# Kernel tuning notes

Hardware: AMD Instinct MI355X
Metric: run time of the kernel (lower is better)

The kernel has to match this reference:

```python
import jax, jax.numpy as jnp
import numpy as np

DIMS = [1536, 2048, 2560, 3072, 1792, 2304, 2816, 2048, 2560, 3328]

def _ln(x, g, b, eps=1e-5):
    m = jnp.mean(x, -1, keepdims=True)
    v = jnp.mean((x - m) ** 2, -1, keepdims=True)
    return (x - m) / jnp.sqrt(v + eps) * g + b

def _gelu(x):
    return jax.nn.gelu(x, approximate=False)

def _mish(x):
    return x * jnp.tanh(jax.nn.softplus(x))

_ACTS = [jax.nn.silu, _gelu, _mish, jax.nn.relu, jax.nn.selu, jnp.tanh, jax.nn.softplus, jax.nn.elu]

def _renorm_sparse_topk(probs, active_k, max_k):
    vals, idx = jax.lax.top_k(probs, max_k)
    mask = (jnp.arange(max_k)[None, :] < active_k[:, None]).astype(probs.dtype)
    n = probs.shape[0]
    sparse = jnp.zeros_like(probs).at[jnp.arange(n)[:, None], idx].set(vals * mask)
    return sparse / jnp.clip(jnp.sum(sparse, -1, keepdims=True), 1e-6, None)

def setup_inputs():
    N, IN, OUT, E, M, S, SUB, DST, INNER, SH = 2048, 1024, 10, 10, 24, 4, 4, 40, 768, 2048
    DMAX = max(DIMS)
    ks = iter(jax.random.split(jax.random.key(0), 80))
    def p(shape, std=0.02):
        return jax.random.normal(next(ks), shape, jnp.float32) * std
    eu = np.zeros((E, DMAX, IN), np.float32)
    ed = np.zeros((E, OUT, DMAX), np.float32)
    for i in range(E):
        d = DIMS[i % len(DIMS)]
        eu[i, :d] = np.asarray(p((d, IN), 0.02))
        ed[i, :, :d] = np.asarray(p((OUT, d), 0.01))
    return {
        'x': jax.random.normal(next(ks), (N, IN), jnp.float32),
        'weight': p((OUT, IN), 0.03), 'bias': p((OUT,), 0.01),
        'shared_up_w': p((SH, IN)), 'shared_down_w': p((OUT, SH), 0.01),
        'shared_norm_g': jnp.ones((OUT,)), 'shared_norm_b': jnp.zeros((OUT,)),
        'shared_scale': jnp.asarray(1.0, jnp.float32),
        'memory_keys': p((M, IN)), 'memory_values_init': p((M, IN)),
        'memory_query_w': p((IN, IN), 0.01), 'memory_out_w': p((OUT, IN), 0.01),
        'mem_wgate_w': p((M, 2 * IN), 0.01), 'mem_wgate_b': jnp.zeros((M,)),
        'mem_wval_w': p((IN, IN), 0.01), 'mem_wval_b': jnp.zeros((IN,)),
        'depth_q_w': p((IN, IN), 0.01), 'depth_k_w': p((IN, IN), 0.01),
        'depth_v_w': p((IN, IN), 0.01), 'depth_out_w': p((OUT, IN), 0.01),
        'cell_ln_g': jnp.ones((S, IN)), 'cell_ln_b': jnp.zeros((S, IN)),
        'cell_fc1_w': p((S, INNER, IN)), 'cell_fc1_b': jnp.zeros((S, INNER)),
        'cell_fc2_w': p((S, IN, INNER)), 'cell_fc2_b': jnp.zeros((S, IN)),
        'ssm_a_w': p((DST, IN), 0.01), 'ssm_a_b': jnp.zeros((DST,)),
        'ssm_b_w': p((IN, DST), 0.01), 'ssm_b_b': jnp.zeros((IN,)),
        'mor_sub_w': p((SUB, E, IN)), 'mor_sub_b': jnp.zeros((SUB, E)),
        'mor_mix_w': p((SUB, IN)), 'mor_mix_b': jnp.zeros((SUB,)),
        'expert_bias': jnp.zeros((E,)),
        'budget_w': p((4, IN)), 'budget_b': jnp.zeros((4,)),
        'experts_up': jnp.asarray(eu), 'experts_down': jnp.asarray(ed),
        'expert_norm_g': jnp.ones((E, OUT)), 'expert_norm_b': jnp.zeros((E, OUT)),
        'halt_w': p((S, 1, IN), 0.01), 'halt_b': jnp.full((S, 1), -2.0, jnp.float32),
        'alpha': jnp.asarray(0.1, jnp.float32), 'beta': jnp.asarray(0.1, jnp.float32),
    }

def reference(x, weight, bias, shared_up_w, shared_down_w, shared_norm_g, shared_norm_b, shared_scale, memory_keys, memory_values_init, memory_query_w, memory_out_w, mem_wgate_w, mem_wgate_b, mem_wval_w, mem_wval_b, depth_q_w, depth_k_w, depth_v_w, depth_out_w, cell_ln_g, cell_ln_b, cell_fc1_w, cell_fc1_b, cell_fc2_w, cell_fc2_b, ssm_a_w, ssm_a_b, ssm_b_w, ssm_b_b, mor_sub_w, mor_sub_b, mor_mix_w, mor_mix_b, expert_bias, budget_w, budget_b, experts_up, experts_down, expert_norm_g, expert_norm_b, halt_w, halt_b, alpha, beta):
    in_dim = x.shape[-1]
    x_flat = x.reshape(-1, in_dim)
    n = x_flat.shape[0]
    base = x_flat @ weight.T + bias
    shared = _ln(jax.nn.silu(x_flat @ shared_up_w.T) @ shared_down_w.T, shared_norm_g, shared_norm_b)
    mem_vals = jnp.broadcast_to(memory_values_init[None], (n,) + memory_values_init.shape)
    current = x_flat
    total = jnp.zeros_like(base)
    cum_halt = jnp.zeros((n, 1), x.dtype)
    bank = []
    mem_scale = in_dim ** -0.5
    steps = cell_ln_g.shape[0]
    n_exp = expert_bias.shape[0]
    max_topk = min(4, n_exp)
    for step in range(steps):
        mq = current @ memory_query_w.T
        mem_attn = jax.nn.softmax((mq @ memory_keys.T) * mem_scale, -1)  # [n, M]
        mem_ctx = jnp.einsum('nm,nmd->nd', mem_attn, mem_vals)
        if bank:
            ds = jnp.stack(bank, 1)  # [n, s, d]
            q = current @ depth_q_w.T
            k = ds @ depth_k_w.T
            v = ds @ depth_v_w.T
            attn = jax.nn.softmax(jnp.einsum('nd,nsd->ns', q, k) * mem_scale, -1)
            depth_ctx = jnp.einsum('ns,nsd->nd', attn, v)
        else:
            depth_ctx = jnp.zeros_like(current)
        ssm_corr = jnp.tanh(current @ ssm_a_w.T + ssm_a_b) @ ssm_b_w.T + ssm_b_b
        enriched = current + 0.34 * mem_ctx + 0.22 * depth_ctx + 0.18 * ssm_corr
        h = _gelu(_ln(enriched, cell_ln_g[step], cell_ln_b[step]) @ cell_fc1_w[step].T + cell_fc1_b[step])
        current = enriched + h @ cell_fc2_w[step].T + cell_fc2_b[step]
        bank.append(current)
        sub = jnp.einsum('nd,sed->nse', current, mor_sub_w) + mor_sub_b[None]
        mix = jax.nn.softmax(current @ mor_mix_w.T + mor_mix_b, -1)
        gate_probs = jax.nn.softmax(jnp.einsum('ns,nse->ne', mix, sub) + expert_bias, -1)
        budget = 1 + jnp.argmax(jax.nn.softmax(current @ budget_w.T + budget_b, -1), -1)
        sg = _renorm_sparse_topk(gate_probs, budget, max_topk)
        expert_logits = jnp.zeros_like(base)
        for i in range(n_exp):
            d = DIMS[i % len(DIMS)]
            hh = _ACTS[i % len(_ACTS)](current @ experts_up[i, :d, :].T)
            eo = _ln(hh @ experts_down[i, :, :d].T, expert_norm_g[i], expert_norm_b[i])
            expert_logits = expert_logits + sg[:, i:i + 1] * eo
        step_logits = expert_logits + 0.22 * (mem_ctx @ memory_out_w.T) + 0.14 * (depth_ctx @ depth_out_w.T)
        surprise = 1.0 - jnp.max(sg, -1, keepdims=True)  # [n, 1]
        wg = jax.nn.softmax(jnp.concatenate([current, mem_ctx], -1) @ mem_wgate_w.T + mem_wgate_b, -1)
        wv = (current @ mem_wval_w.T + mem_wval_b)[:, None, :]
        mem_vals = mem_vals + surprise[..., None] * wg[..., None] * (wv - mem_vals)
        halt = jax.nn.sigmoid((current + 0.2 * mem_ctx + 0.1 * depth_ctx) @ halt_w[step].T + halt_b[step])
        remaining = 1.0 - cum_halt
        total = total + remaining * step_logits
        cum_halt = cum_halt + remaining * halt
    total = total / float(steps)
    out = base + shared_scale * shared + (alpha + 1e-4) * total + beta * (current @ memory_out_w.T)
    return out.reshape(x.shape[:-1] + (out.shape[-1],))
```

## Files before the change

### kernel.cpp

```cpp
#include <hip/hip_runtime.h>
#include <stdint.h>

#define N_TOK 2048
#define IN_D  1024
#define NEXP  10
#define NSTEP 4
#define INNER 768
#define SHD   2048
#define DMAX  3328
#define DSUM  24064

typedef __attribute__((ext_vector_type(4))) float f32x4;
typedef __attribute__((ext_vector_type(8))) short bf16x8;

__device__ const int c_dims[10] = {1536,2048,2560,3072,1792,2304,2816,2048,2560,3328};
__device__ const int c_offs[10] = {0,1536,3584,6144,9216,11008,13312,16128,18176,20736};
__device__ const int c_acts[10] = {0,1,2,3,4,5,6,7,0,1};
__device__ const int c_cum[11]  = {0,12,28,48,72,86,104,126,142,162,188};

__device__ __forceinline__ float wred(float v){
#pragma unroll
  for (int s = 32; s > 0; s >>= 1) v += __shfl_xor(v, s, 64);
  return v;
}
__device__ __forceinline__ float wmax(float v){
#pragma unroll
  for (int s = 32; s > 0; s >>= 1) v = fmaxf(v, __shfl_xor(v, s, 64));
  return v;
}
__device__ __forceinline__ float bf2f(uint16_t u){
  return __uint_as_float(((uint32_t)u) << 16);
}
__device__ __forceinline__ uint16_t f2bf(float f){
  uint32_t u = __float_as_uint(f);
  return (uint16_t)((u + 0x7FFFu + ((u >> 16) & 1u)) >> 16);
}
__device__ __forceinline__ uint8_t f2fp8(float f){
  uint32_t u = __float_as_uint(f);
  uint8_t sign = (uint8_t)((u >> 24) & 0x80u);
  uint32_t absu = u & 0x7FFFFFFFu;
  if (absu >= 0x43E00000u) return sign | 0x7Eu;
  if (absu < 0x3C800000u){
    float af = __uint_as_float(absu);
    int q = (int)rintf(af * 512.0f);
    return sign | (uint8_t)q;
  }
  uint32_t mant = absu & 0x7FFFFFu;
  uint32_t exp = absu >> 23;
  uint32_t lsb = (mant >> 20) & 1u;
  uint32_t rounded = mant + 0x7FFFFu + lsb;
  if (rounded >= 0x800000u){ exp += 1; rounded = 0; }
  uint32_t e8 = exp - 120;
  uint32_t m8 = (rounded >> 20) & 7u;
  if (e8 > 15u || (e8 == 15u && m8 == 7u)) return sign | 0x7Eu;
  return sign | (uint8_t)((e8 << 3) | m8);
}
__device__ __forceinline__ void gload16(const uint16_t* g, uint16_t* l){
  __builtin_amdgcn_global_load_lds(
      (const __attribute__((address_space(1))) uint32_t*)(const void*)g,
      (__attribute__((address_space(3))) uint32_t*)(void*)l, 16, 0, 0);
}
__device__ __forceinline__ void gload16b(const void* g, void* l){
  __builtin_amdgcn_global_load_lds(
      (const __attribute__((address_space(1))) uint32_t*)g,
      (__attribute__((address_space(3))) uint32_t*)l, 16, 0, 0);
}

__device__ __forceinline__ float actf(int a, float x){
  switch(a){
    case 0: return x / (1.f + expf(-x));
    case 1: return 0.5f * x * (1.f + erff(x * 0.7071067811865475f));
    case 2: { float sp = fmaxf(x,0.f) + log1pf(expf(-fabsf(x)));
              return x * tanhf(sp); }
    case 3: return fmaxf(x, 0.f);
    case 4: return x > 0.f ? 1.0507009873554805f * x
                           : 1.7580993408473768f * expm1f(x);
    case 5: return tanhf(x);
    case 6: return fmaxf(x,0.f) + log1pf(expf(-fabsf(x)));
    default: return x > 0.f ? x : expm1f(x);
  }
}

__global__ void split_kernel(const float* __restrict__ src, uint16_t* __restrict__ hi,
                             uint16_t* __restrict__ lo, size_t n){
  size_t i = ((size_t)blockIdx.x * blockDim.x + threadIdx.x) << 2;
  size_t stride = ((size_t)gridDim.x * blockDim.x) << 2;
  for (; i < n; i += stride){
    float4 v = *(const float4*)(src + i);
    ushort4 h, l;
    h.x = f2bf(v.x); l.x = f2bf(v.x - bf2f(h.x));
    h.y = f2bf(v.y); l.y = f2bf(v.y - bf2f(h.y));
    h.z = f2bf(v.z); l.z = f2bf(v.z - bf2f(h.z));
    h.w = f2bf(v.w); l.w = f2bf(v.w - bf2f(h.w));
    *(ushort4*)(hi + i) = h;
    *(ushort4*)(lo + i) = l;
  }
}
__global__ void split_strided(const float* __restrict__ src, uint16_t* __restrict__ hi,
                              uint16_t* __restrict__ lo, int rows, int cols, int ldd){
  int nq = rows * (cols >> 2);
  for (int i = blockIdx.x * blockDim.x + threadIdx.x; i < nq; i += gridDim.x * blockDim.x){
    int r = i / (cols >> 2), c4 = (i - r * (cols >> 2)) << 2;
    float4 v = *(const float4*)(src + (size_t)r * cols + c4);
    ushort4 h, l;
    h.x = f2bf(v.x); l.x = f2bf(v.x - bf2f(h.x));
    h.y = f2bf(v.y); l.y = f2bf(v.y - bf2f(h.y));
    h.z = f2bf(v.z); l.z = f2bf(v.z - bf2f(h.z));
    h.w = f2bf(v.w); l.w = f2bf(v.w - bf2f(h.w));
    size_t d = (size_t)r * ldd + c4;
    *(ushort4*)(hi + d) = h;
    *(ushort4*)(lo + d) = l;
  }
}
__global__ void cvt_fp8_kernel(const float* __restrict__ src, uint8_t* __restrict__ dst, size_t n){
  size_t i = ((size_t)blockIdx.x * blockDim.x + threadIdx.x) << 2;
  size_t stride = ((size_t)gridDim.x * blockDim.x) << 2;
  for (; i < n; i += stride){
    float4 v = *(const float4*)(src + i);
    uchar4 q;
    q.x = f2fp8(v.x); q.y = f2fp8(v.y); q.z = f2fp8(v.z); q.w = f2fp8(v.w);
    *(uchar4*)(dst + i) = q;
  }
}
__global__ void fill1_kernel(float* __restrict__ p, int n){
  int i = blockIdx.x * blockDim.x + threadIdx.x;
  if (i < n) p[i] = 1.f;
}
__global__ void tr_sbw_kernel(const float* __restrict__ src, float* __restrict__ dst){
  int i = blockIdx.x * 256 + threadIdx.x;
  if (i < 40 * 1024){
    int o = i >> 10, d = i & 1023;
    dst[i] = src[d * 40 + o];
  }
}

__global__ __launch_bounds__(256)
void k2_kernel(const float* __restrict__ keys, const float* __restrict__ mqw,
               float* __restrict__ K2){
  int m = blockIdx.x;
  int j = blockIdx.y * 256 + threadIdx.x;
  float acc = 0.f;
  for (int d = 0; d < 1024; d++)
    acc = fmaf(keys[m * 1024 + d], mqw[d * 1024 + j], acc);
  K2[m * 1024 + j] = acc;
}

__global__ void build_routew(const float* __restrict__ msw, const float* __restrict__ mmw,
                             const float* __restrict__ bw, const float* __restrict__ wgw,
                             const float* __restrict__ hw, const float* __restrict__ mow,
                             const float* __restrict__ dow, uint16_t* __restrict__ Wh,
                             uint16_t* __restrict__ Wl){
  const int TOT = 4 * 128 * 3072;
  for (int i = blockIdx.x * 256 + threadIdx.x; i < TOT; i += gridDim.x * 256){
    int t = i / (128 * 3072);
    int rem = i - t * (128 * 3072);
    int row = rem / 3072, col = rem - row * 3072;
    float v = 0.f;
    if (row < 40){ if (col < 1024) v = msw[row * 1024 + col]; }
    else if (row < 44){ if (col < 1024) v = mmw[(row - 40) * 1024 + col]; }
    else if (row < 48){ if (col < 1024) v = bw[(row - 44) * 1024 + col]; }
    else if (row < 72){ if (col < 2048) v = wgw[(row - 48) * 2048 + col]; }
    else if (row == 72){
      if (col < 1024) v = hw[t * 1024 + col];
      else if (col < 2048) v = 0.2f * hw[t * 1024 + col - 1024];
      else v = 0.1f * hw[t * 1024 + col - 2048];
    }
    else if (row < 83){ if (col >= 1024 && col < 2048) v = mow[(row - 73) * 1024 + col - 1024]; }
    else if (row < 93){ if (col >= 2048) v = dow[(row - 83) * 1024 + col - 2048]; }
    else if (row < 103){ if (col < 1024) v = mow[(row - 93) * 1024 + col]; }
    uint16_t h = f2bf(v);
    Wh[i] = h; Wl[i] = f2bf(v - bf2f(h));
  }
}

enum { EPI_GELU=0, EPI_CUR=1, EPI_PRE=2, EPI_QROUTE=3 };

template<int EPI>
__global__ __launch_bounds__(256)
void gemm_sp(const uint16_t* __restrict__ Ah, const uint16_t* __restrict__ Al, int lda,
             const uint16_t* __restrict__ Wh, const uint16_t* __restrict__ Wl,
             const uint16_t* __restrict__ W2h, const uint16_t* __restrict__ W2l,
             const float* __restrict__ bias, const float* __restrict__ addend,
             float* __restrict__ D0, float* __restrict__ D1, float* __restrict__ D2,
             float* __restrict__ D3, uint8_t* __restrict__ o8,
             uint16_t* __restrict__ oH, uint16_t* __restrict__ oL,
             int K, int D)
{
  __shared__ __align__(16) uint16_t sm[4][2][4096];
  int tid = threadIdx.x, lane = tid & 63, wave = tid >> 6;
  int wr = wave >> 1, wc = wave & 1;
  int arow = lane & 15, agrp = lane >> 4;
  int rowBase = blockIdx.y * 128;
  bool isRoute = (EPI == EPI_QROUTE) && ((int)blockIdx.x < 4);
  const uint16_t* Wsh = isRoute ? W2h : Wh;
  const uint16_t* Wsl = isRoute ? W2l : Wl;
  int wst     = isRoute ? 3072 : K;
  int colBase = isRoute ? 0 : ((EPI == EPI_QROUTE ? (int)blockIdx.x - 4 : (int)blockIdx.x) * 128);
  int kBase   = isRoute ? (int)blockIdx.x * 768 : 0;
  int kLen    = isRoute ? 768 : K;
  f32x4 acc[4][4];
#pragma unroll
  for (int m = 0; m < 4; m++)
#pragma unroll
    for (int n = 0; n < 4; n++){ f32x4 z = {0.f,0.f,0.f,0.f}; acc[m][n] = z; }

#define STAGE_G(buf, k0) do { \
  _Pragma("unroll") \
  for (int s = 0; s < 2; s++){ \
    int u = tid + s * 256; \
    int rr = u >> 2; \
    int ch = (u & 3) ^ ((rr >> 1) & 3); \
    size_t ga = (size_t)(rowBase + rr) * lda + kBase + (k0) + ch * 8; \
    size_t gw = (size_t)(colBase + rr) * wst + kBase + (k0) + ch * 8; \
    gload16(&Ah[ga], &sm[0][buf][u << 3]); \
    gload16(&Al[ga], &sm[1][buf][u << 3]); \
    gload16(&Wsh[gw], &sm[2][buf][u << 3]); \
    gload16(&Wsl[gw], &sm[3][buf][u << 3]); \
  } } while(0)

  int nk = kLen >> 5;
  STAGE_G(0, 0);
  if (nk > 1) STAGE_G(1, 32);
  int perm = (arow >> 1) & 3;
#pragma unroll 1
  for (int ki = 0; ki < nk; ki++){
    int cb = ki & 1;
    if (ki + 1 < nk) asm volatile("s_waitcnt vmcnt(8)" ::: "memory");
    else             asm volatile("s_waitcnt vmcnt(0)" ::: "memory");
    __builtin_amdgcn_s_barrier();
    bf16x8 ah[4], al[4], bh[4], bl[4];
#pragma unroll
    for (int m = 0; m < 4; m++){
      int u = ((wr*64 + m*16 + arow) << 2) + (agrp ^ perm);
      ah[m] = *(const bf16x8*)&sm[0][cb][u << 3];
      al[m] = *(const bf16x8*)&sm[1][cb][u << 3];
    }
#pragma unroll
    for (int n = 0; n < 4; n++){
      int u = ((wc*64 + n*16 + arow) << 2) + (agrp ^ perm);
      bh[n] = *(const bf16x8*)&sm[2][cb][u << 3];
      bl[n] = *(const bf16x8*)&sm[3][cb][u << 3];
    }
#pragma unroll
    for (int m = 0; m < 4; m++)
#pragma unroll
      for (int n = 0; n < 4; n++){
        acc[m][n] = __builtin_amdgcn_mfma_f32_16x16x32_bf16(ah[m], bh[n], acc[m][n], 0, 0, 0);
        acc[m][n] = __builtin_amdgcn_mfma_f32_16x16x32_bf16(ah[m], bl[n], acc[m][n], 0, 0, 0);
        acc[m][n] = __builtin_amdgcn_mfma_f32_16x16x32_bf16(al[m], bh[n], acc[m][n], 0, 0, 0);
      }
    __builtin_amdgcn_s_barrier();
    asm volatile("" ::: "memory");
    if (ki + 2 < nk) STAGE_G(cb, (ki + 2) << 5);
  }
#undef STAGE_G
#pragma unroll
  for (int m = 0; m < 4; m++){
#pragma unroll
    for (int n = 0; n < 4; n++){
      int col = colBase + wc*64 + n*16 + arow;
#pragma unroll
      for (int r2 = 0; r2 < 4; r2++){
        int row = rowBase + wr*64 + m*16 + agrp*4 + r2;
        float v = acc[m][n][r2];
        if (EPI == EPI_GELU){
          v += bias[col];
          v = 0.5f * v * (1.f + erff(v * 0.7071067811865475f));
          size_t idx = (size_t)row * D + col;
          uint16_t h = f2bf(v); oH[idx] = h; oL[idx] = f2bf(v - bf2f(h));
        }
        if (EPI == EPI_CUR){
          v += bias[col] + addend[(size_t)row * 1024 + col];
          D0[(size_t)row * 1024 + col] = v;
          size_t idx = (size_t)row * 3072 + col;
          uint16_t h = f2bf(v); oH[idx] = h; oL[idx] = f2bf(v - bf2f(h));
          o8[(size_t)row * 1024 + col] = f2fp8(v);
        }
        if (EPI == EPI_PRE){
          if (col < 2048) D0[(size_t)row * 2048 + col] = v / (1.f + expf(-v));
          else D1[(size_t)row * 128 + col - 2048] = v;
        }
        if (EPI == EPI_QROUTE){
          if (isRoute){
            D3[((size_t)blockIdx.x * N_TOK + row) * 128 + col] = v;
          } else {
            if (col < 1024) D0[(size_t)row * 1024 + col] = v;
            else if (col < 4096) D1[(size_t)row * 3072 + col - 1024] = v + bias[col - 1024];
            else if (col < 4160) D2[(size_t)row * 128 + col - 4096] = v;
          }
        }
      }
    }
  }
}

__global__ __launch_bounds__(256)
void expert_up_mfma(const uint8_t* __restrict__ A8, const uint8_t* __restrict__ U8,
                    const int* __restrict__ cnt, const int* __restrict__ gidx,
                    uint16_t* __restrict__ HH)
{
  int bid = blockIdx.x;
  int ex = bid / 192;
  int ey = bid - ex * 192;
  if (ey >= 188) return;
  int e = 0;
#pragma unroll
  for (int i = 1; i < 11; i++) if (ey >= c_cum[i]) e = i;
  int ct = ey - c_cum[e];
  int dcols = c_dims[e];
  int ne = cnt[e];
  const uint8_t* W = U8 + (size_t)e * DMAX * IN_D + (size_t)ct * 128 * IN_D;

  __shared__ __align__(16) uint8_t smem[32768];
  int tid = threadIdx.x, lane = tid & 63, wave = tid >> 6;
  int wr = wave >> 1, wc = wave & 1;
  int arow = lane & 15, agrp = lane >> 4;
  int actid = c_acts[e];
  size_t base_e = (size_t)N_TOK * c_offs[e];
  int rHalf = tid >> 1;
  int h16 = (((tid & 1) ^ ((tid >> 3) & 1)) << 4);
  int off = ((((agrp >> 1) ^ ((arow >> 2) & 1)) << 4) | ((agrp & 1) << 3));

#define STAGE_E(b, k0) do { \
    gload16b(&A8[(size_t)tok * IN_D + (k0) + h16], &smem[(b)*8192 + tid*16]); \
    gload16b(&W[(size_t)rHalf * IN_D + (k0) + h16], &smem[(b)*8192 + 4096 + tid*16]); \
  } while(0)

#pragma unroll 1
  for (int rowBase = ex * 128; rowBase < ne; rowBase += 4 * 128){
    int slot = rowBase + rHalf;
    int tok = (slot < ne) ? gidx[e * N_TOK + slot] : 0;

    f32x4 acc[4][4];
#pragma unroll
    for (int m = 0; m < 4; m++)
#pragma unroll
      for (int n = 0; n < 4; n++){ f32x4 z = {0.f,0.f,0.f,0.f}; acc[m][n] = z; }

    STAGE_E(0, 0);
    STAGE_E(1, 32);
    STAGE_E(2, 64);
    int cb = 0;
#pragma unroll 1
    for (int ki = 0; ki < 32; ki++){
      if (ki < 30)       asm volatile("s_waitcnt vmcnt(4)" ::: "memory");
      else if (ki == 30) asm volatile("s_waitcnt vmcnt(2)" ::: "memory");
      else               asm volatile("s_waitcnt vmcnt(0)" ::: "memory");
      __builtin_amdgcn_s_barrier();
      long a[4], b[4];
#pragma unroll
      for (int m = 0; m < 4; m++)
        a[m] = *(const long*)&smem[cb*8192 + (wr*64 + m*16 + arow)*32 + off];
#pragma unroll
      for (int n = 0; n < 4; n++)
        b[n] = *(const long*)&smem[cb*8192 + 4096 + (wc*64 + n*16 + arow)*32 + off];
#pragma unroll
      for (int m = 0; m < 4; m++)
#pragma unroll
        for (int n = 0; n < 4; n++)
          acc[m][n] = __builtin_amdgcn_mfma_f32_16x16x32_fp8_fp8(a[m], b[n], acc[m][n], 0, 0, 0);
      __builtin_amdgcn_s_barrier();
      asm volatile("" ::: "memory");
      if (ki + 3 < 32) STAGE_E(cb, (ki + 3) << 5);
      cb = (cb == 2) ? 0 : cb + 1;
    }
    uint16_t* Ht = (uint16_t*)smem;
#pragma unroll
    for (int m = 0; m < 4; m++){
      int rb0 = wr*64 + m*16 + agrp*4;
#pragma unroll
      for (int n = 0; n < 4; n++){
        int col = wc*64 + n*16 + arow;
#pragma unroll
        for (int r2 = 0; r2 < 4; r2++){
          int row = rb0 + r2;
          float v = actf(actid, acc[m][n][r2]);
          Ht[row * 128 + (col ^ ((row & 7) << 3))] = f2bf(v);
        }
      }
    }
    __syncthreads();
#pragma unroll
    for (int i = 0; i < 8; i++){
      int c = tid + i * 256;
      int row = c >> 4, chunk = c & 15;
      int schunk = (chunk & 8) | ((chunk ^ row) & 7);
      int4 val = *(const int4*)&Ht[row * 128 + schunk * 8];
      *(int4*)&HH[base_e + (size_t)(rowBase + row) * dcols
                  + (size_t)ct * 128 + chunk * 8] = val;
    }
    __syncthreads();
  }
#undef STAGE_E
}

__global__ __launch_bounds__(256)
void ctx_enr_kernel(const float* __restrict__ qaux, const float* __restrict__ dqbuf,
                    const float* __restrict__ Ac, const float* __restrict__ W0,
                    const float* __restrict__ W1, const float* __restrict__ W2,
                    const float* __restrict__ mvi,
                    const float* __restrict__ t0, const float* __restrict__ t1,
                    const float* __restrict__ t2, const float* __restrict__ cur,
                    const float* __restrict__ sab, const float* __restrict__ sbwT,
                    const float* __restrict__ sbb, const float* __restrict__ lng,
                    const float* __restrict__ lnbv,
                    float* __restrict__ enr, uint16_t* __restrict__ lnh,
                    uint16_t* __restrict__ lnl, uint16_t* __restrict__ Arh,
                    uint16_t* __restrict__ Arl, int t)
{
  int row = blockIdx.x, tid = threadIdx.x;
  __shared__ float su[24], ss[3], s40[40], red[12], redm[8];
  if (tid < 64){
    float pj = (tid < 24) ? qaux[(size_t)row * 128 + tid] * 0.03125f : -1e30f;
    float mx = wmax(pj);
    float ex = (tid < 24) ? expf(pj - mx) : 0.f;
    float sum = wred(ex);
    float attn = ex / sum;
    if (tid < 24) su[tid] = attn * Ac[row * 24 + tid];
    float w0v = (t > 0 && tid < 24) ? W0[row * 24 + tid] : 0.f;
    float s0 = wred(attn * w0v);
    float w1v = (t > 1 && tid < 24) ? W1[row * 24 + tid] : 0.f;
    float s1 = wred(attn * w1v);
    float w2v = (t > 2 && tid < 24) ? W2[row * 24 + tid] : 0.f;
    float s2 = wred(attn * w2v);
    if (tid == 0){ ss[0] = s0; ss[1] = s1; ss[2] = s2; }
    if (tid < 40) s40[tid] = tanhf(qaux[(size_t)row * 128 + 24 + tid] + sab[tid]);
  }
  size_t tb = (size_t)row * 3072;
  if (t > 0){
    float a0 = 0.f, a1 = 0.f, a2 = 0.f;
#pragma unroll
    for (int j = 0; j < 4; j++){
      int d = tid + j * 256;
      float dq = dqbuf[(size_t)row * 1024 + d];
      a0 = fmaf(dq, t0[tb + d], a0);
      if (t > 1) a1 = fmaf(dq, t1[tb + d], a1);
      if (t > 2) a2 = fmaf(dq, t2[tb + d], a2);
    }
    a0 = wred(a0); a1 = wred(a1); a2 = wred(a2);
    if ((tid & 63) == 0){ int w = tid >> 6; red[w] = a0; red[4+w] = a1; red[8+w] = a2; }
  }
  __syncthreads();
  float e0 = 0.f, e1 = 0.f, e2 = 0.f;
  if (t > 0){
    float A0 = (red[0]+red[1]+red[2]+red[3]) * 0.03125f;
    float A1 = (red[4]+red[5]+red[6]+red[7]) * 0.03125f;
    float A2 = (red[8]+red[9]+red[10]+red[11]) * 0.03125f;
    float dmx = A0;
    if (t > 1) dmx = fmaxf(dmx, A1);
    if (t > 2) dmx = fmaxf(dmx, A2);
    e0 = expf(A0 - dmx);
    e1 = (t > 1) ? expf(A1 - dmx) : 0.f;
    e2 = (t > 2) ? expf(A2 - dmx) : 0.f;
    float dinv = 1.f / (e0 + e1 + e2);
    e0 *= dinv; e1 *= dinv; e2 *= dinv;
  }
  size_t ar = (size_t)row * 3072;
  float ev[4];
  float part = 0.f;
#pragma unroll
  for (int j = 0; j < 4; j++){
    int d = tid + j * 256;
    size_t idx = (size_t)row * IN_D + d;
    float mv = 0.f;
#pragma unroll
    for (int m = 0; m < 24; m++) mv = fmaf(su[m], mvi[m * IN_D + d], mv);
    float dv = 0.f;
    if (t > 0){
      mv = fmaf(ss[0], t0[tb + 2048 + d], mv);
      dv = e0 * t0[tb + 1024 + d];
      if (t > 1){ mv = fmaf(ss[1], t1[tb + 2048 + d], mv); dv = fmaf(e1, t1[tb + 1024 + d], dv); }
      if (t > 2){ mv = fmaf(ss[2], t2[tb + 2048 + d], mv); dv = fmaf(e2, t2[tb + 1024 + d], dv); }
    }
    float sv = sbb[d];
#pragma unroll
    for (int o = 0; o < 40; o++) sv = fmaf(s40[o], sbwT[o * 1024 + d], sv);
    float v = cur[idx] + 0.34f * mv + 0.22f * dv + 0.18f * sv;
    uint16_t mh = f2bf(mv);
    Arh[ar + 1024 + d] = mh; Arl[ar + 1024 + d] = f2bf(mv - bf2f(mh));
    uint16_t dh = f2bf(dv);
    Arh[ar + 2048 + d] = dh; Arl[ar + 2048 + d] = f2bf(dv - bf2f(dh));
    ev[j] = v; part += v;
  }
  part = wred(part);
  if ((tid & 63) == 0) redm[tid >> 6] = part;
  __syncthreads();
  float mean = (redm[0] + redm[1] + redm[2] + redm[3]) * (1.f / 1024.f);
  float vp = 0.f;
#pragma unroll
  for (int j = 0; j < 4; j++){ float dd = ev[j] - mean; vp += dd * dd; }
  vp = wred(vp);
  if ((tid & 63) == 0) redm[4 + (tid >> 6)] = vp;
  __syncthreads();
  float var = (redm[4] + redm[5] + redm[6] + redm[7]) * (1.f / 1024.f);
  float rs = 1.f / sqrtf(var + 1e-5f);
#pragma unroll
  for (int j = 0; j < 4; j++){
    int d = tid + j * 256;
    size_t idx = (size_t)row * IN_D + d;
    enr[idx] = ev[j];
    float v = (ev[j] - mean) * rs * lng[t * IN_D + d] + lnbv[t * IN_D + d];
    uint16_t h = f2bf(v);
    lnh[idx] = h;
    lnl[idx] = f2bf(v - bf2f(h));
  }
}

__global__ __launch_bounds__(256)
void route_fin(const float* __restrict__ ROq, const float* __restrict__ mmb,
               const float* __restrict__ msb, const float* __restrict__ ebias,
               const float* __restrict__ bb, const float* __restrict__ wgb,
               const float* __restrict__ hb,
               float* __restrict__ sg, float* __restrict__ haltb,
               float* __restrict__ Ac, float* __restrict__ W0,
               float* __restrict__ W1, float* __restrict__ W2,
               int* __restrict__ cnt, int* __restrict__ gidx,
               int* __restrict__ pos, float* __restrict__ routeS, int t)
{
  int row = blockIdx.x * 256 + threadIdx.x;
  int lane = threadIdx.x & 63;
  const size_t P = (size_t)N_TOK * 128;
  const float* r0 = ROq + (size_t)row * 128;
  const float* r1 = r0 + P;
  const float* r2 = r0 + 2 * P;
  const float* r3 = r0 + 3 * P;
  auto R = [&](int j){ return r0[j] + r1[j] + r2[j] + r3[j]; };
  float pm[4];
#pragma unroll
  for (int o = 0; o < 4; o++) pm[o] = R(40 + o) + mmb[o];
  float mmx = fmaxf(fmaxf(pm[0], pm[1]), fmaxf(pm[2], pm[3]));
  float msum = 0.f;
#pragma unroll
  for (int o = 0; o < 4; o++){ pm[o] = expf(pm[o] - mmx); msum += pm[o]; }
  float minv = 1.f / msum;
  float gl[10];
#pragma unroll
  for (int e = 0; e < 10; e++){
    float g = ebias[e];
#pragma unroll
    for (int s2 = 0; s2 < 4; s2++)
      g = fmaf(pm[s2] * minv, R(s2 * 10 + e) + msb[s2 * 10 + e], g);
    gl[e] = g;
  }
  float gmx = gl[0];
#pragma unroll
  for (int e = 1; e < 10; e++) gmx = fmaxf(gmx, gl[e]);
  float gs = 0.f;
#pragma unroll
  for (int e = 0; e < 10; e++){ gl[e] = expf(gl[e] - gmx); gs += gl[e]; }
  float ginv = 1.f / gs;
#pragma unroll
  for (int e = 0; e < 10; e++) gl[e] *= ginv;
  float pb0 = R(44) + bb[0], pb1 = R(45) + bb[1], pb2 = R(46) + bb[2], pb3 = R(47) + bb[3];
  int bud = 1; float bbest = pb0;
  if (pb1 > bbest){ bbest = pb1; bud = 2; }
  if (pb2 > bbest){ bbest = pb2; bud = 3; }
  if (pb3 > bbest){ bbest = pb3; bud = 4; }
  float tv[4]; int ti[4]; unsigned used = 0;
#pragma unroll
  for (int j = 0; j < 4; j++){
    float best = -1e30f; int bi = 0;
#pragma unroll
    for (int e = 0; e < 10; e++){
      bool ok = (!((used >> e) & 1u)) && (gl[e] > best);
      if (ok){ best = gl[e]; bi = e; }
    }
    tv[j] = best; ti[j] = bi; used |= (1u << bi);
  }
  float ssum = tv[0];
  if (bud > 1) ssum += tv[1];
  if (bud > 2) ssum += tv[2];
  if (bud > 3) ssum += tv[3];
  float den = fmaxf(ssum, 1e-6f);
  float sup = 1.f - tv[0] / den;
  float sgv[10];
#pragma unroll
  for (int e = 0; e < 10; e++){
    float sv = 0.f;
#pragma unroll
    for (int j = 0; j < 4; j++) if (j < bud && ti[j] == e) sv = tv[j] / den;
    sgv[e] = sv;
    sg[row * 10 + e] = sv;
  }
  float pw[24];
#pragma unroll
  for (int m = 0; m < 24; m++) pw[m] = R(48 + m) + wgb[m];
  float wmx2 = pw[0];
#pragma unroll
  for (int m = 1; m < 24; m++) wmx2 = fmaxf(wmx2, pw[m]);
  float wsum = 0.f;
#pragma unroll
  for (int m = 0; m < 24; m++){ pw[m] = expf(pw[m] - wmx2); wsum += pw[m]; }
  float winv = 1.f / wsum;
#pragma unroll
  for (int m = 0; m < 24; m++){
    float c = sup * pw[m] * winv;
    float om = 1.f - c;
    Ac[row * 24 + m] *= om;
    if (t > 0) W0[row * 24 + m] *= om;
    if (t > 1) W1[row * 24 + m] *= om;
    if (t > 2) W2[row * 24 + m] *= om;
    if (t == 0)      W0[row * 24 + m] = c;
    else if (t == 1) W1[row * 24 + m] = c;
    else if (t == 2) W2[row * 24 + m] = c;
  }
  haltb[row] = 1.f / (1.f + expf(-(R(72) + hb[t])));
#pragma unroll
  for (int i = 0; i < 30; i++) routeS[row * 32 + i] = R(73 + i);
#pragma unroll
  for (int e = 0; e < 10; e++){
    bool act = sgv[e] != 0.f;
    unsigned long long mask = __ballot(act);
    int cw = __popcll(mask);
    int b0 = 0;
    if (lane == 0 && cw > 0) b0 = atomicAdd(&cnt[e], cw);
    b0 = __shfl(b0, 0, 64);
    if (act){
      int slot = b0 + __popcll(mask & ((1ull << lane) - 1ull));
      gidx[e * N_TOK + slot] = row;
      pos[row * 10 + e] = slot;
    }
  }
}

__global__ __launch_bounds__(256)
void downfin_kernel(const uint16_t* __restrict__ HH, const int* __restrict__ pos,
                    const float* __restrict__ ED, const float* __restrict__ sg,
                    const float* __restrict__ eng, const float* __restrict__ enb,
                    const float* __restrict__ routeS, const float* __restrict__ haltb,
                    float* __restrict__ total, float* __restrict__ cumh)
{
  int lane = threadIdx.x & 63;
  int row = blockIdx.x * 4 + (threadIdx.x >> 6);
  float out[10] = {};
  for (int e = 0; e < NEXP; e++){
    float g = sg[row * 10 + e];
    if (g != 0.0f){
      int d = c_dims[e];
      int slot = pos[row * 10 + e];
      const uint16_t* hr = HH + (size_t)N_TOK * c_offs[e] + (size_t)slot * d;
      const float* wd = ED + (size_t)e * 10 * DMAX;
      float p[10] = {};
      for (int k = lane * 4; k < d; k += 256){
        uint2 hv = *(const uint2*)&hr[k];
        float h0 = bf2f((uint16_t)hv.x), h1 = bf2f((uint16_t)(hv.x >> 16));
        float h2 = bf2f((uint16_t)hv.y), h3 = bf2f((uint16_t)(hv.y >> 16));
#pragma unroll
        for (int o = 0; o < 10; o++){
          float4 w4 = *(const float4*)&wd[o * DMAX + k];
          p[o] = fmaf(h0, w4.x, fmaf(h1, w4.y, fmaf(h2, w4.z, fmaf(h3, w4.w, p[o]))));
        }
      }
#pragma unroll
      for (int o = 0; o < 10; o++) p[o] = wred(p[o]);
      float mean = 0.f;
#pragma unroll
      for (int o = 0; o < 10; o++) mean += p[o];
      mean *= 0.1f;
      float var = 0.f;
#pragma unroll
      for (int o = 0; o < 10; o++){ float dd = p[o] - mean; var += dd * dd; }
      var *= 0.1f;
      float rs = 1.f / sqrtf(var + 1e-5f);
#pragma unroll
      for (int o = 0; o < 10; o++)
        out[o] += g * ((p[o] - mean) * rs * eng[e * 10 + o] + enb[e * 10 + o]);
    }
  }
  if (lane == 0){
    const float* r = routeS + (size_t)row * 32;
    float rem = 1.f - cumh[row];
#pragma unroll
    for (int o = 0; o < 10; o++)
      total[row * 10 + o] += rem * (out[o] + 0.22f * r[o] + 0.14f * r[10 + o]);
    cumh[row] += rem * haltb[row];
  }
}

__global__ __launch_bounds__(256)
void shared_kernel(const float* __restrict__ shpre, const float* __restrict__ sdw,
                   const float* __restrict__ g, const float* __restrict__ b,
                   float* __restrict__ outp)
{
  int lane = threadIdx.x & 63;
  int row = blockIdx.x * 4 + (threadIdx.x >> 6);
  const float* xr = shpre + (size_t)row * SHD;
  float p[10];
#pragma unroll
  for (int o = 0; o < 10; o++) p[o] = 0.f;
  for (int k = lane; k < SHD; k += 64){
    float xv = xr[k];
#pragma unroll
    for (int o = 0; o < 10; o++) p[o] = fmaf(xv, sdw[o * SHD + k], p[o]);
  }
#pragma unroll
  for (int o = 0; o < 10; o++) p[o] = wred(p[o]);
  float mean = 0.f;
#pragma unroll
  for (int o = 0; o < 10; o++) mean += p[o];
  mean *= 0.1f;
  float var = 0.f;
#pragma unroll
  for (int o = 0; o < 10; o++){ float dd = p[o] - mean; var += dd * dd; }
  var *= 0.1f;
  float rs = 1.f / sqrtf(var + 1e-5f);
  if (lane == 0){
#pragma unroll
    for (int o = 0; o < 10; o++) outp[row * 10 + o] = (p[o] - mean) * rs * g[o] + b[o];
  }
}

__global__ __launch_bounds__(256)
void final_lite(const float* __restrict__ qaux, const float* __restrict__ biasp,
                const float* __restrict__ sharedp, const float* __restrict__ total,
                const float* __restrict__ routeS, const float* __restrict__ sscale,
                const float* __restrict__ alphap, const float* __restrict__ betap,
                float* __restrict__ outp)
{
  int row = blockIdx.x * 256 + threadIdx.x;
  float ss = sscale[0], av = alphap[0] + 1e-4f, bv = betap[0];
#pragma unroll
  for (int o = 0; o < 10; o++)
    outp[row * 10 + o] = (qaux[(size_t)row * 128 + 64 + o] + biasp[o])
                       + ss * sharedp[row * 10 + o]
                       + av * (total[row * 10 + o] * 0.25f)
                       + bv * routeS[(size_t)row * 32 + 20 + o];
}

extern "C" void kernel_launch(void* const* d_in, const int* in_sizes, int n_in,
                              void* d_out, int out_size, void* d_ws, size_t ws_size,
                              hipStream_t stream)
{
  const float* x     = (const float*)d_in[0];
  const float* wgt   = (const float*)d_in[1];
  const float* bias  = (const float*)d_in[2];
  const float* suw   = (const float*)d_in[3];
  const float* sdw   = (const float*)d_in[4];
  const float* sng   = (const float*)d_in[5];
  const float* snb   = (const float*)d_in[6];
  const float* sscale= (const float*)d_in[7];
  const float* keys  = (const float*)d_in[8];
  const float* mvi   = (const float*)d_in[9];
  const float* mqw   = (const float*)d_in[10];
  const float* mow   = (const float*)d_in[11];
  const float* wgw   = (const float*)d_in[12];
  const float* wgb   = (const float*)d_in[13];
  const float* wvw   = (const float*)d_in[14];
  const float* wvb   = (const float*)d_in[15];
  const float* dqw   = (const float*)d_in[16];
  const float* dkw   = (const float*)d_in[17];
  const float* dvw   = (const float*)d_in[18];
  const float* dow   = (const float*)d_in[19];
  const float* clng  = (const float*)d_in[20];
  const float* clnb  = (const float*)d_in[21];
  const float* fc1w  = (const float*)d_in[22];
  const float* fc1b  = (const float*)d_in[23];
  const float* fc2w  = (const float*)d_in[24];
  const float* fc2b  = (const float*)d_in[25];
  const float* saw   = (const float*)d_in[26];
  const float* sab   = (const float*)d_in[27];
  const float* sbw   = (const float*)d_in[28];
  const float* sbb   = (const float*)d_in[29];
  const float* msw   = (const float*)d_in[30];
  const float* msb   = (const float*)d_in[31];
  const float* mmw   = (const float*)d_in[32];
  const float* mmb   = (const float*)d_in[33];
  const float* ebias = (const float*)d_in[34];
  const float* bw    = (const float*)d_in[35];
  const float* bb    = (const float*)d_in[36];
  const float* eup   = (const float*)d_in[37];
  const float* edn   = (const float*)d_in[38];
  const float* eng   = (const float*)d_in[39];
  const float* enb   = (const float*)d_in[40];
  const float* hw    = (const float*)d_in[41];
  const float* hb    = (const float*)d_in[42];
  const float* alphap= (const float*)d_in[43];
  const float* betap = (const float*)d_in[44];
  float* outp = (float*)d_out;

  char* wsb = (char*)d_ws;
  size_t off = 0;
  auto AL = [&](size_t bytes) -> void* {
    void* p = wsb + off;
    off = (off + bytes + 255) & ~(size_t)255;
    return p;
  };
  const size_t NI = (size_t)N_TOK * IN_D;
  float* cur    = (float*)AL(NI * 4);
  float* enr    = (float*)AL(NI * 4);
  float* dqbuf  = (float*)AL(NI * 4);
  float* qaux   = (float*)AL((size_t)N_TOK * 128 * 4);
  float* routeQ = (float*)AL((size_t)4 * N_TOK * 128 * 4);
  float* routeS = (float*)AL((size_t)N_TOK * 32 * 4);
  float* trio0  = (float*)AL((size_t)N_TOK * 3072 * 4);
  float* trio1  = (float*)AL((size_t)N_TOK * 3072 * 4);
  float* trio2  = (float*)AL((size_t)N_TOK * 3072 * 4);
  float* Ac     = (float*)AL((size_t)N_TOK * 24 * 4);
  float* W0     = (float*)AL((size_t)N_TOK * 24 * 4);
  float* W1     = (float*)AL((size_t)N_TOK * 24 * 4);
  float* W2     = (float*)AL((size_t)N_TOK * 24 * 4);
  float* sg     = (float*)AL((size_t)N_TOK * 10 * 4);
  float* haltb  = (float*)AL((size_t)N_TOK * 4);
  char*  zblk   = (char*)AL((size_t)N_TOK * 10 * 4 + N_TOK * 4 + 4 * 16 * 4);
  float* total  = (float*)zblk;
  float* cumh   = (float*)(zblk + (size_t)N_TOK * 10 * 4);
  int*   cnt    = (int*)(zblk + (size_t)N_TOK * 10 * 4 + N_TOK * 4);
  int*   gidx   = (int*)AL((size_t)NEXP * N_TOK * 4);
  int*   pos    = (int*)AL((size_t)N_TOK * NEXP * 4);
  float* sharedp= (float*)AL((size_t)N_TOK * 10 * 4);
  float* cbias  = (float*)AL(3072 * 4);
  float* K2f    = (float*)AL((size_t)24 * 1024 * 4);
  float* sbwT   = (float*)AL((size_t)40 * 1024 * 4);
  uint16_t* lnh  = (uint16_t*)AL(NI * 2);
  uint16_t* lnl  = (uint16_t*)AL(NI * 2);
  uint16_t* h7h  = (uint16_t*)AL((size_t)N_TOK * INNER * 2);
  uint16_t* h7l  = (uint16_t*)AL((size_t)N_TOK * INNER * 2);
  uint16_t* Arh  = (uint16_t*)AL((size_t)N_TOK * 3072 * 2);
  uint16_t* Arl  = (uint16_t*)AL((size_t)N_TOK * 3072 * 2);
  const size_t W1M = (size_t)IN_D * IN_D;
  uint16_t* preWh  = (uint16_t*)AL((size_t)2176 * 1024 * 2);
  uint16_t* preWl  = (uint16_t*)AL((size_t)2176 * 1024 * 2);
  uint16_t* qtWh   = (uint16_t*)AL((size_t)4224 * 1024 * 2);
  uint16_t* qtWl   = (uint16_t*)AL((size_t)4224 * 1024 * 2);
  uint16_t* rtWh   = (uint16_t*)AL((size_t)4 * 128 * 3072 * 2);
  uint16_t* rtWl   = (uint16_t*)AL((size_t)4 * 128 * 3072 * 2);
  const size_t WFC = (size_t)NSTEP * INNER * IN_D;
  uint16_t* fc1wh = (uint16_t*)AL(WFC * 2); uint16_t* fc1wl = (uint16_t*)AL(WFC * 2);
  uint16_t* fc2wh = (uint16_t*)AL(WFC * 2); uint16_t* fc2wl = (uint16_t*)AL(WFC * 2);
  uint8_t* upbf8 = (uint8_t*)AL((size_t)NEXP * DMAX * IN_D);
  uint8_t* A8    = (uint8_t*)AL(NI);
  uint16_t* HHc  = (uint16_t*)AL((size_t)N_TOK * DSUM * 2);
  float* shpre  = (float*)HHc;

  hipMemsetAsync(zblk, 0, (size_t)N_TOK * 10 * 4 + N_TOK * 4 + 4 * 16 * 4, stream);
  hipMemsetAsync(cbias, 0, 3072 * 4, stream);
  hipMemcpyAsync(cbias + 2048, wvb, 1024 * 4, hipMemcpyDeviceToDevice, stream);
  hipMemcpyAsync(cur, x, NI * 4, hipMemcpyDeviceToDevice, stream);
  fill1_kernel<<<(N_TOK * 24 + 255) / 256, 256, 0, stream>>>(Ac, N_TOK * 24);
  cvt_fp8_kernel<<<2048, 256, 0, stream>>>(eup, upbf8, (size_t)NEXP * DMAX * IN_D);
  tr_sbw_kernel<<<160, 256, 0, stream>>>(sbw, sbwT);

  split_strided<<<1024, 256, 0, stream>>>(x, Arh, Arl, N_TOK, 1024, 3072);
  split_kernel<<<1024, 256, 0, stream>>>(suw, preWh, preWl, (size_t)SHD * 1024);
  split_kernel<<<256, 256, 0, stream>>>(saw, preWh + (size_t)2072*1024, preWl + (size_t)2072*1024, (size_t)40 * 1024);
  split_kernel<<<256, 256, 0, stream>>>(wgt, preWh + (size_t)2112*1024, preWl + (size_t)2112*1024, (size_t)10 * 1024);
  hipMemsetAsync(preWh + (size_t)2122*1024, 0, (size_t)54 * 1024 * 2, stream);
  hipMemsetAsync(preWl + (size_t)2122*1024, 0, (size_t)54 * 1024 * 2, stream);
  split_kernel<<<1024, 256, 0, stream>>>(dqw, qtWh, qtWl, W1M);
  split_kernel<<<1024, 256, 0, stream>>>(dkw, qtWh + W1M, qtWl + W1M, W1M);
  split_kernel<<<1024, 256, 0, stream>>>(dvw, qtWh + 2*W1M, qtWl + 2*W1M, W1M);
  split_kernel<<<1024, 256, 0, stream>>>(wvw, qtWh + 3*W1M, qtWl + 3*W1M, W1M);
  split_kernel<<<256, 256, 0, stream>>>(saw, qtWh + (size_t)4120*1024, qtWl + (size_t)4120*1024, (size_t)40 * 1024);
  hipMemsetAsync(qtWh + (size_t)4160*1024, 0, (size_t)64 * 1024 * 2, stream);
  hipMemsetAsync(qtWl + (size_t)4160*1024, 0, (size_t)64 * 1024 * 2, stream);
  k2_kernel<<<dim3(24, 4), 256, 0, stream>>>(keys, mqw, K2f);
  split_kernel<<<256, 256, 0, stream>>>(K2f, preWh + (size_t)2048*1024, preWl + (size_t)2048*1024, (size_t)24 * 1024);
  split_kernel<<<256, 256, 0, stream>>>(K2f, qtWh + (size_t)4096*1024, qtWl + (size_t)4096*1024, (size_t)24 * 1024);
  build_routew<<<2048, 256, 0, stream>>>(msw, mmw, bw, wgw, hw, mow, dow, rtWh, rtWl);
  split_kernel<<<1024, 256, 0, stream>>>(fc1w, fc1wh, fc1wl, WFC);
  split_kernel<<<1024, 256, 0, stream>>>(fc2w, fc2wh, fc2wl, WFC);

  gemm_sp<EPI_PRE><<<dim3(17, 16), 256, 0, stream>>>(
      Arh, Arl, 3072, preWh, preWl, nullptr, nullptr, nullptr, nullptr,
      shpre, qaux, nullptr, nullptr, nullptr, nullptr, nullptr, IN_D, 2176);
  shared_kernel<<<512, 256, 0, stream>>>(shpre, sdw, sng, snb, sharedp);

  float* trioB[3] = {trio0, trio1, trio2};

  for (int t = 0; t < NSTEP; t++){
    ctx_enr_kernel<<<2048, 256, 0, stream>>>(qaux, dqbuf, Ac, W0, W1, W2, mvi,
                                             trio0, trio1, trio2, cur, sab, sbwT, sbb,
                                             clng, clnb, enr, lnh, lnl, Arh, Arl, t);
    gemm_sp<EPI_GELU><<<dim3(INNER/128, 16), 256, 0, stream>>>(
        lnh, lnl, 1024, fc1wh + (size_t)t * INNER * IN_D, fc1wl + (size_t)t * INNER * IN_D,
        nullptr, nullptr, fc1b + t * INNER, nullptr,
        nullptr, nullptr, nullptr, nullptr, nullptr, h7h, h7l, IN_D, INNER);
    gemm_sp<EPI_CUR><<<dim3(8, 16), 256, 0, stream>>>(
        h7h, h7l, 768, fc2wh + (size_t)t * IN_D * INNER, fc2wl + (size_t)t * IN_D * INNER,
        nullptr, nullptr, fc2b + t * IN_D, enr,
        cur, nullptr, nullptr, nullptr, A8, Arh, Arl, INNER, IN_D);
    gemm_sp<EPI_QROUTE><<<dim3(t < 3 ? 37 : 4, 16), 256, 0, stream>>>(
        Arh, Arl, 3072, qtWh, qtWl,
        rtWh + (size_t)t * 128 * 3072, rtWl + (size_t)t * 128 * 3072,
        cbias, nullptr, dqbuf, t < 3 ? trioB[t] : nullptr, qaux, routeQ,
        nullptr, nullptr, nullptr, IN_D, 4224);
    route_fin<<<8, 256, 0, stream>>>(routeQ, mmb, msb, ebias, bb, wgb, hb,
                                     sg, haltb, Ac, W0, W1, W2,
                                     cnt + t * 16, gidx, pos, routeS, t);
    expert_up_mfma<<<768, 256, 0, stream>>>(A8, upbf8, cnt + t * 16, gidx, HHc);
    downfin_kernel<<<512, 256, 0, stream>>>(HHc, pos, edn, sg, eng, enb,
                                            routeS, haltb, total, cumh);
  }
  final_lite<<<8, 256, 0, stream>>>(qaux, bias, sharedp, total, routeS,
                                    sscale, alphap, betap, outp);
}
```

Measured before the change: 2.076 ms.

## Process four rows per block in ctx_enr to reuse memory-value and side weights

The context-enrichment kernel now handles four token rows per 256-thread block, with one wave per row for the softmax and depth-attention scalars. Each loaded element of mvi and sbwT feeds four rows, so the shared weight reads drop to a quarter. Per-row values are staged in a 16 KB shared buffer for the layernorm pass. The cost is fewer blocks (512 instead of 2048) and more shared memory per block, which may lower occupancy and latency hiding in a kernel that is a small part of total time.

```diff
diff --git a/kernel.cpp b/kernel.cpp
--- a/kernel.cpp
+++ b/kernel.cpp
@@ -408,101 +408,133 @@
                     uint16_t* __restrict__ lnl, uint16_t* __restrict__ Arh,
                     uint16_t* __restrict__ Arl, int t)
 {
-  int row = blockIdx.x, tid = threadIdx.x;
-  __shared__ float su[24], ss[3], s40[40], red[12], redm[8];
-  if (tid < 64){
-    float pj = (tid < 24) ? qaux[(size_t)row * 128 + tid] * 0.03125f : -1e30f;
+  int row0 = blockIdx.x * 4;
+  int tid = threadIdx.x, lane = tid & 63, wave = tid >> 6;
+  int roww = row0 + wave;
+  __shared__ float su[4][24], ss[4][3], de[4][3], s40[4][40], redm[4][8];
+  __shared__ float sev[4][1024];
+  {
+    float pj = (lane < 24) ? qaux[(size_t)roww * 128 + lane] * 0.03125f : -1e30f;
     float mx = wmax(pj);
-    float ex = (tid < 24) ? expf(pj - mx) : 0.f;
+    float ex = (lane < 24) ? expf(pj - mx) : 0.f;
     float sum = wred(ex);
     float attn = ex / sum;
-    if (tid < 24) su[tid] = attn * Ac[row * 24 + tid];
-    float w0v = (t > 0 && tid < 24) ? W0[row * 24 + tid] : 0.f;
+    if (lane < 24) su[wave][lane] = attn * Ac[roww * 24 + lane];
+    float w0v = (t > 0 && lane < 24) ? W0[roww * 24 + lane] : 0.f;
     float s0 = wred(attn * w0v);
-    float w1v = (t > 1 && tid < 24) ? W1[row * 24 + tid] : 0.f;
+    float w1v = (t > 1 && lane < 24) ? W1[roww * 24 + lane] : 0.f;
     float s1 = wred(attn * w1v);
-    float w2v = (t > 2 && tid < 24) ? W2[row * 24 + tid] : 0.f;
+    float w2v = (t > 2 && lane < 24) ? W2[roww * 24 + lane] : 0.f;
     float s2 = wred(attn * w2v);
-    if (tid == 0){ ss[0] = s0; ss[1] = s1; ss[2] = s2; }
-    if (tid < 40) s40[tid] = tanhf(qaux[(size_t)row * 128 + 24 + tid] + sab[tid]);
-  }
-  size_t tb = (size_t)row * 3072;
+    if (lane == 0){ ss[wave][0] = s0; ss[wave][1] = s1; ss[wave][2] = s2; }
+    if (lane < 40) s40[wave][lane] = tanhf(qaux[(size_t)roww * 128 + 24 + lane] + sab[lane]);
+  }
   if (t > 0){
+    size_t tbw = (size_t)roww * 3072;
     float a0 = 0.f, a1 = 0.f, a2 = 0.f;
-#pragma unroll
-    for (int j = 0; j < 4; j++){
-      int d = tid + j * 256;
-      float dq = dqbuf[(size_t)row * 1024 + d];
-      a0 = fmaf(dq, t0[tb + d], a0);
-      if (t > 1) a1 = fmaf(dq, t1[tb + d], a1);
-      if (t > 2) a2 = fmaf(dq, t2[tb + d], a2);
-    }
-    a0 = wred(a0); a1 = wred(a1); a2 = wred(a2);
-    if ((tid & 63) == 0){ int w = tid >> 6; red[w] = a0; red[4+w] = a1; red[8+w] = a2; }
-  }
+    for (int d = lane; d < 1024; d += 64){
+      float dq = dqbuf[(size_t)roww * 1024 + d];
+      a0 = fmaf(dq, t0[tbw + d], a0);
+      if (t > 1) a1 = fmaf(dq, t1[tbw + d], a1);
+      if (t > 2) a2 = fmaf(dq, t2[tbw + d], a2);
+    }
+    a0 = wred(a0) * 0.03125f; a1 = wred(a1) * 0.03125f; a2 = wred(a2) * 0.03125f;
+    float dmx = a0;
+    if (t > 1) dmx = fmaxf(dmx, a1);
+    if (t > 2) dmx = fmaxf(dmx, a2);
+    float e0 = expf(a0 - dmx);
+    float e1 = (t > 1) ? expf(a1 - dmx) : 0.f;
+    float e2 = (t > 2) ? expf(a2 - dmx) : 0.f;
+    float dinv = 1.f / (e0 + e1 + e2);
+    if (lane == 0){ de[wave][0] = e0 * dinv; de[wave][1] = e1 * dinv; de[wave][2] = e2 * dinv; }
+  } else if (lane == 0){ de[wave][0] = 0.f; de[wave][1] = 0.f; de[wave][2] = 0.f; }
   __syncthreads();
-  float e0 = 0.f, e1 = 0.f, e2 = 0.f;
-  if (t > 0){
-    float A0 = (red[0]+red[1]+red[2]+red[3]) * 0.03125f;
-    float A1 = (red[4]+red[5]+red[6]+red[7]) * 0.03125f;
-    float A2 = (red[8]+red[9]+red[10]+red[11]) * 0.03125f;
-    float dmx = A0;
-    if (t > 1) dmx = fmaxf(dmx, A1);
-    if (t > 2) dmx = fmaxf(dmx, A2);
-    e0 = expf(A0 - dmx);
-    e1 = (t > 1) ? expf(A1 - dmx) : 0.f;
-    e2 = (t > 2) ? expf(A2 - dmx) : 0.f;
-    float dinv = 1.f / (e0 + e1 + e2);
-    e0 *= dinv; e1 *= dinv; e2 *= dinv;
-  }
-  size_t ar = (size_t)row * 3072;
-  float ev[4];
-  float part = 0.f;
-#pragma unroll
+  float part0 = 0.f, part1 = 0.f, part2 = 0.f, part3 = 0.f;
+#pragma unroll 1
   for (int j = 0; j < 4; j++){
     int d = tid + j * 256;
-    size_t idx = (size_t)row * IN_D + d;
-    float mv = 0.f;
-#pragma unroll
-    for (int m = 0; m < 24; m++) mv = fmaf(su[m], mvi[m * IN_D + d], mv);
-    float dv = 0.f;
-    if (t > 0){
-      mv = fmaf(ss[0], t0[tb + 2048 + d], mv);
-      dv = e0 * t0[tb + 1024 + d];
-      if (t > 1){ mv = fmaf(ss[1], t1[tb + 2048 + d], mv); dv = fmaf(e1, t1[tb + 1024 + d], dv); }
-      if (t > 2){ mv = fmaf(ss[2], t2[tb + 2048 + d], mv); dv = fmaf(e2, t2[tb + 1024 + d], dv); }
-    }
-    float sv = sbb[d];
-#pragma unroll
-    for (int o = 0; o < 40; o++) sv = fmaf(s40[o], sbwT[o * 1024 + d], sv);
-    float v = cur[idx] + 0.34f * mv + 0.22f * dv + 0.18f * sv;
-    uint16_t mh = f2bf(mv);
-    Arh[ar + 1024 + d] = mh; Arl[ar + 1024 + d] = f2bf(mv - bf2f(mh));
-    uint16_t dh = f2bf(dv);
-    Arh[ar + 2048 + d] = dh; Arl[ar + 2048 + d] = f2bf(dv - bf2f(dh));
-    ev[j] = v; part += v;
-  }
-  part = wred(part);
-  if ((tid & 63) == 0) redm[tid >> 6] = part;
+    float mv[4] = {0.f,0.f,0.f,0.f};
+    float sv[4] = {0.f,0.f,0.f,0.f};
+#pragma unroll 8
+    for (int m = 0; m < 24; m++){
+      float w = mvi[m * 1024 + d];
+#pragma unroll
+      for (int r = 0; r < 4; r++) mv[r] = fmaf(su[r][m], w, mv[r]);
+    }
+#pragma unroll 8
+    for (int o = 0; o < 40; o++){
+      float w = sbwT[o * 1024 + d];
+#pragma unroll
+      for (int r = 0; r < 4; r++) sv[r] = fmaf(s40[r][o], w, sv[r]);
+    }
+    float sbbv = sbb[d];
+#pragma unroll
+    for (int r = 0; r < 4; r++){
+      int row = row0 + r;
+      size_t tb = (size_t)row * 3072;
+      float mvr = mv[r], dvr = 0.f;
+      if (t > 0){
+        mvr = fmaf(ss[r][0], t0[tb + 2048 + d], mvr);
+        dvr = de[r][0] * t0[tb + 1024 + d];
+        if (t > 1){ mvr = fmaf(ss[r][1], t1[tb + 2048 + d], mvr); dvr = fmaf(de[r][1], t1[tb + 1024 + d], dvr); }
+        if (t > 2){ mvr = fmaf(ss[r][2], t2[tb + 2048 + d], mvr); dvr = fmaf(de[r][2], t2[tb + 1024 + d], dvr); }
+      }
+      float v = cur[(size_t)row * 1024 + d] + 0.34f * mvr + 0.22f * dvr
+              + 0.18f * (sbbv + sv[r]);
+      size_t ar = (size_t)row * 3072;
+      uint16_t mh = f2bf(mvr);
+      Arh[ar + 1024 + d] = mh; Arl[ar + 1024 + d] = f2bf(mvr - bf2f(mh));
+      uint16_t dh = f2bf(dvr);
+      Arh[ar + 2048 + d] = dh; Arl[ar + 2048 + d] = f2bf(dvr - bf2f(dh));
+      sev[r][d] = v;
+      if (r == 0) part0 += v; else if (r == 1) part1 += v;
+      else if (r == 2) part2 += v; else part3 += v;
+    }
+  }
+  {
+    float p0 = wred(part0), p1 = wred(part1), p2 = wred(part2), p3 = wred(part3);
+    if (lane == 0){ redm[0][wave] = p0; redm[1][wave] = p1; redm[2][wave] = p2; redm[3][wave] = p3; }
+  }
   __syncthreads();
-  float mean = (redm[0] + redm[1] + redm[2] + redm[3]) * (1.f / 1024.f);
-  float vp = 0.f;
-#pragma unroll
-  for (int j = 0; j < 4; j++){ float dd = ev[j] - mean; vp += dd * dd; }
-  vp = wred(vp);
-  if ((tid & 63) == 0) redm[4 + (tid >> 6)] = vp;
-  __syncthreads();
-  float var = (redm[4] + redm[5] + redm[6] + redm[7]) * (1.f / 1024.f);
-  float rs = 1.f / sqrtf(var + 1e-5f);
+  float mean0 = (redm[0][0]+redm[0][1]+redm[0][2]+redm[0][3]) * (1.f/1024.f);
+  float mean1 = (redm[1][0]+redm[1][1]+redm[1][2]+redm[1][3]) * (1.f/1024.f);
+  float mean2 = (redm[2][0]+redm[2][1]+redm[2][2]+redm[2][3]) * (1.f/1024.f);
+  float mean3 = (redm[3][0]+redm[3][1]+redm[3][2]+redm[3][3]) * (1.f/1024.f);
+  float vp0 = 0.f, vp1 = 0.f, vp2 = 0.f, vp3 = 0.f;
 #pragma unroll
   for (int j = 0; j < 4; j++){
     int d = tid + j * 256;
-    size_t idx = (size_t)row * IN_D + d;
-    enr[idx] = ev[j];
-    float v = (ev[j] - mean) * rs * lng[t * IN_D + d] + lnbv[t * IN_D + d];
-    uint16_t h = f2bf(v);
-    lnh[idx] = h;
-    lnl[idx] = f2bf(v - bf2f(h));
+    float d0 = sev[0][d] - mean0; vp0 = fmaf(d0, d0, vp0);
+    float d1 = sev[1][d] - mean1; vp1 = fmaf(d1, d1, vp1);
+    float d2 = sev[2][d] - mean2; vp2 = fmaf(d2, d2, vp2);
+    float d3 = sev[3][d] - mean3; vp3 = fmaf(d3, d3, vp3);
+  }
+  {
+    float p0 = wred(vp0), p1 = wred(vp1), p2 = wred(vp2), p3 = wred(vp3);
+    if (lane == 0){ redm[0][4+wave] = p0; redm[1][4+wave] = p1; redm[2][4+wave] = p2; redm[3][4+wave] = p3; }
+  }
+  __syncthreads();
+  float rs0 = 1.f / sqrtf((redm[0][4]+redm[0][5]+redm[0][6]+redm[0][7]) * (1.f/1024.f) + 1e-5f);
+  float rs1 = 1.f / sqrtf((redm[1][4]+redm[1][5]+redm[1][6]+redm[1][7]) * (1.f/1024.f) + 1e-5f);
+  float rs2 = 1.f / sqrtf((redm[2][4]+redm[2][5]+redm[2][6]+redm[2][7]) * (1.f/1024.f) + 1e-5f);
+  float rs3 = 1.f / sqrtf((redm[3][4]+redm[3][5]+redm[3][6]+redm[3][7]) * (1.f/1024.f) + 1e-5f);
+#pragma unroll 1
+  for (int j = 0; j < 4; j++){
+    int d = tid + j * 256;
+    float lg = lng[t * 1024 + d], lb = lnbv[t * 1024 + d];
+    float mean[4] = {mean0, mean1, mean2, mean3};
+    float rs[4] = {rs0, rs1, rs2, rs3};
+#pragma unroll
+    for (int r = 0; r < 4; r++){
+      int row = row0 + r;
+      size_t idx = (size_t)row * 1024 + d;
+      float v0 = sev[r][d];
+      enr[idx] = v0;
+      float v = (v0 - mean[r]) * rs[r] * lg + lb;
+      uint16_t h = f2bf(v);
+      lnh[idx] = h;
+      lnl[idx] = f2bf(v - bf2f(h));
+    }
   }
 }
 
@@ -868,9 +900,9 @@
   float* trioB[3] = {trio0, trio1, trio2};
 
   for (int t = 0; t < NSTEP; t++){
-    ctx_enr_kernel<<<2048, 256, 0, stream>>>(qaux, dqbuf, Ac, W0, W1, W2, mvi,
-                                             trio0, trio1, trio2, cur, sab, sbwT, sbb,
-                                             clng, clnb, enr, lnh, lnl, Arh, Arl, t);
+    ctx_enr_kernel<<<512, 256, 0, stream>>>(qaux, dqbuf, Ac, W0, W1, W2, mvi,
+                                            trio0, trio1, trio2, cur, sab, sbwT, sbb,
+                                            clng, clnb, enr, lnh, lnl, Arh, Arl, t);
     gemm_sp<EPI_GELU><<<dim3(INNER/128, 16), 256, 0, stream>>>(
         lnh, lnl, 1024, fc1wh + (size_t)t * INNER * IN_D, fc1wl + (size_t)t * INNER * IN_D,
         nullptr, nullptr, fc1b + t * INNER, nullptr,
```

Result: faster. 1.783 ms (-14.1%).
